# Performance work log

Hardware: AMD Instinct MI355X
Metric: run time of the kernel (lower is better)

The kernel has to match this reference:

```python
import jax, jax.numpy as jnp
import numpy as np

B, L, D, P = 2, 1024, 256, 32

def setup_inputs() -> dict:
    key = jax.random.key(0)
    k1, k2, k3, k4, k5 = jax.random.split(key, 5)
    x = jax.random.normal(k1, (B, L, D), dtype=jnp.float32)
    s_in = 1.0 / np.sqrt(D)
    W_phase = jax.random.normal(k2, (D, P), dtype=jnp.float32) * s_in
    b_phase = jax.random.normal(k3, (P,), dtype=jnp.float32) * 0.01
    W_val = jax.random.normal(k4, (D, D), dtype=jnp.float32) * s_in
    b_val = jax.random.normal(k5, (D,), dtype=jnp.float32) * 0.01
    return {"x": x, "W_phase": W_phase, "b_phase": b_phase, "W_val": W_val, "b_val": b_val}

def reference(x, W_phase, b_phase, W_val, b_val):
    # phases: [B, L, P] in (-pi, pi)
    phases = jnp.tanh(x @ W_phase + b_phase) * jnp.float32(np.pi)
    # unit-magnitude complex phasors: [B, L, P]
    phasors = jnp.exp(1j * phases)  # complex64
    # values: [B, L, D]
    values = x @ W_val + b_val
    # bind value vector to each phasor via outer product: [B, L, P, D] complex64
    bound = phasors[..., None] * values[:, :, None, :].astype(jnp.complex64)
    # holographic memory = running sum over sequence position
    memory = jnp.cumsum(bound, axis=1)
    return (memory, phases, phasors)
```

## Files before the change

kernel.cpp:

```cpp
#include <hip/hip_runtime.h>
#include <math.h>

#define B_ 2
#define L_ 1024
#define D_ 256
#define P_ 32
#define NROW (B_*L_)
#define C_ 16
#define CL_ (L_/C_)
#define PIF 3.14159265358979323846f

typedef float nvf4 __attribute__((ext_vector_type(4)));
typedef float nvf2 __attribute__((ext_vector_type(2)));

__global__ __launch_bounds__(256) void k_proj3(
    const float* __restrict__ x, const float* __restrict__ Wp,
    const float* __restrict__ bp, const float* __restrict__ Wv,
    const float* __restrict__ bv, float* __restrict__ values,
    float* __restrict__ phases_out, float* __restrict__ phasor_out,
    float* __restrict__ phasorT, int phasorMode, int mode, int hasPT)
{
    __shared__ float smem[2560];
    const int tid = threadIdx.x;

    if (blockIdx.x < NROW / 2) {
        const int row0 = blockIdx.x * 2;
        float*  xsv = smem;
        float4* red = (float4*)(smem + 512);

        if (tid < 128)
            ((float4*)xsv)[tid] = ((const float4*)(x + (size_t)row0 * D_))[tid];
        __syncthreads();

        const int q  = tid >> 6;
        const int c4 = tid & 63;
        const float4* Wv4 = (const float4*)Wv;
        float4 acc0 = make_float4(0.f, 0.f, 0.f, 0.f);
        float4 acc1 = make_float4(0.f, 0.f, 0.f, 0.f);

        const int k0 = q * 64;
        for (int kk = 0; kk < 64; kk += 4) {
            const int k = k0 + kk;
            float4 w0 = Wv4[(k + 0) * 64 + c4];
            float4 w1 = Wv4[(k + 1) * 64 + c4];
            float4 w2 = Wv4[(k + 2) * 64 + c4];
            float4 w3 = Wv4[(k + 3) * 64 + c4];
            float4 xa = *(const float4*)(xsv + 0 * D_ + k);
            float4 xb = *(const float4*)(xsv + 1 * D_ + k);
            acc0.x += xa.x*w0.x + xa.y*w1.x + xa.z*w2.x + xa.w*w3.x;
            acc0.y += xa.x*w0.y + xa.y*w1.y + xa.z*w2.y + xa.w*w3.y;
            acc0.z += xa.x*w0.z + xa.y*w1.z + xa.z*w2.z + xa.w*w3.z;
            acc0.w += xa.x*w0.w + xa.y*w1.w + xa.z*w2.w + xa.w*w3.w;
            acc1.x += xb.x*w0.x + xb.y*w1.x + xb.z*w2.x + xb.w*w3.x;
            acc1.y += xb.x*w0.y + xb.y*w1.y + xb.z*w2.y + xb.w*w3.y;
            acc1.z += xb.x*w0.z + xb.y*w1.z + xb.z*w2.z + xb.w*w3.z;
            acc1.w += xb.x*w0.w + xb.y*w1.w + xb.z*w2.w + xb.w*w3.w;
        }
        red[(0 * 4 + q) * 64 + c4] = acc0;
        red[(1 * 4 + q) * 64 + c4] = acc1;
        __syncthreads();

        if (tid < 128) {
            const int r2 = tid >> 6;
            const int cb = tid & 63;
            float4 s0 = red[(r2 * 4 + 0) * 64 + cb];
            float4 s1 = red[(r2 * 4 + 1) * 64 + cb];
            float4 s2 = red[(r2 * 4 + 2) * 64 + cb];
            float4 s3 = red[(r2 * 4 + 3) * 64 + cb];
            const float4 b4 = ((const float4*)bv)[cb];
            float4 o;
            o.x = s0.x + s1.x + s2.x + s3.x + b4.x;
            o.y = s0.y + s1.y + s2.y + s3.y + b4.y;
            o.z = s0.z + s1.z + s2.z + s3.z + b4.z;
            o.w = s0.w + s1.w + s2.w + s3.w + b4.w;
            ((float4*)values)[(size_t)(row0 + r2) * 64 + cb] = o;
        }
    } else {
        const int row0 = (blockIdx.x - NROW / 2) * 8;
        float* xs = smem;
        const float4* xg4 = (const float4*)(x + (size_t)row0 * D_);
        ((float4*)xs)[tid]       = xg4[tid];
        ((float4*)xs)[tid + 256] = xg4[tid + 256];
        __syncthreads();

        const int p  = tid & (P_ - 1);
        const int rr = tid >> 5;
        const float* xr = xs + rr * D_;
        float a0 = 0.f, a1 = 0.f, a2 = 0.f, a3 = 0.f;
        for (int k = 0; k < D_; k += 8) {
            float w0 = Wp[(k + 0) * P_ + p];
            float w1 = Wp[(k + 1) * P_ + p];
            float w2 = Wp[(k + 2) * P_ + p];
            float w3 = Wp[(k + 3) * P_ + p];
            float w4 = Wp[(k + 4) * P_ + p];
            float w5 = Wp[(k + 5) * P_ + p];
            float w6 = Wp[(k + 6) * P_ + p];
            float w7 = Wp[(k + 7) * P_ + p];
            float4 xA = *(const float4*)(xr + k);
            float4 xB = *(const float4*)(xr + k + 4);
            a0 += xA.x * w0; a1 += xA.y * w1; a2 += xA.z * w2; a3 += xA.w * w3;
            a0 += xB.x * w4; a1 += xB.y * w5; a2 += xB.z * w6; a3 += xB.w * w7;
        }
        float a = (a0 + a1) + (a2 + a3) + bp[p];
        float e  = __expf(2.0f * a);
        float ph = (1.0f - __fdividef(2.0f, e + 1.0f)) * PIF;
        const int row = row0 + rr;
        const int idx = row * P_ + p;
        phases_out[idx] = ph;
        float s, c;
        __sincosf(ph, &s, &c);
        if (phasorMode == 0) {
            ((float2*)phasor_out)[idx] = make_float2(c, s);
        } else if (phasorMode == 1) {
            phasor_out[idx] = c;
        }
        if (hasPT) {
            const int b = row >> 10, l = row & (L_ - 1);
            const size_t ti = (size_t)(b * P_ + p) * L_ + l;
            if (mode == 1) phasorT[ti] = c;
            else ((float2*)phasorT)[ti] = make_float2(c, s);
        }
    }
}

__global__ __launch_bounds__(128) void k_partial(
    const float* __restrict__ values, const float* __restrict__ phases,
    const float* __restrict__ phasorT, float* __restrict__ S,
    int mode, int hasPT)
{
    const int blk = blockIdx.x;
    const int c = blk & (C_ - 1);
    const int p = (blk >> 4) & (P_ - 1);
    const int b = blk >> 9;
    const int tid = threadIdx.x;
    const int l0 = c * CL_;
    const int bp = b * P_ + p;

    __shared__ float pcs[2 * CL_];
    if (hasPT) {
        if (mode == 1) {
            if (tid < CL_ / 4)
                ((float4*)pcs)[tid] =
                    ((const float4*)(phasorT + (size_t)bp * L_ + l0))[tid];
        } else {
            if (tid < CL_ / 2)
                ((float4*)pcs)[tid] = ((const float4*)
                    ((const float2*)phasorT + (size_t)bp * L_ + l0))[tid];
        }
    } else {
        if (tid < CL_) {
            float ph = phases[(b * L_ + l0 + tid) * P_ + p];
            if (mode == 1) pcs[tid] = __cosf(ph);
            else ((float2*)pcs)[tid] = make_float2(__cosf(ph), __sinf(ph));
        }
    }
    __syncthreads();

    const float2* vp = (const float2*)(values + (size_t)(b * L_ + l0) * D_) + tid;

    if (mode == 1) {
        float sx = 0.f, sy = 0.f;
        #pragma unroll
        for (int i = 0; i < CL_; ++i) {
            float pc = pcs[i];
            float2 v = vp[(size_t)i * (D_/2)];
            sx += pc * v.x;
            sy += pc * v.y;
        }
        ((float2*)S)[((size_t)bp * C_ + c) * (D_/2) + tid] = make_float2(sx, sy);
    } else {
        float4 a = make_float4(0.f, 0.f, 0.f, 0.f);
        #pragma unroll
        for (int i = 0; i < CL_; ++i) {
            float2 q = ((float2*)pcs)[i];
            float2 v = vp[(size_t)i * (D_/2)];
            a.x += q.x * v.x; a.y += q.y * v.x;
            a.z += q.x * v.y; a.w += q.y * v.y;
        }
        ((float4*)S)[((size_t)bp * C_ + c) * (D_/2) + tid] = a;
    }
}

__global__ __launch_bounds__(128) void k_scan(
    const float* __restrict__ values, const float* __restrict__ phases,
    const float* __restrict__ phasorT, const float* __restrict__ S,
    float* __restrict__ mem, int mode, int hasPT)
{
    const int blk = blockIdx.x;
    const int c = blk & (C_ - 1);
    const int p = (blk >> 4) & (P_ - 1);
    const int b = blk >> 9;
    const int tid = threadIdx.x;
    const int l0 = c * CL_;
    const int bp = b * P_ + p;

    __shared__ float pcs[2 * CL_];
    if (hasPT) {
        if (mode == 1) {
            if (tid < CL_ / 4)
                ((float4*)pcs)[tid] =
                    ((const float4*)(phasorT + (size_t)bp * L_ + l0))[tid];
        } else {
            if (tid < CL_ / 2)
                ((float4*)pcs)[tid] = ((const float4*)
                    ((const float2*)phasorT + (size_t)bp * L_ + l0))[tid];
        }
    } else {
        if (tid < CL_) {
            float ph = phases[(b * L_ + l0 + tid) * P_ + p];
            if (mode == 1) pcs[tid] = __cosf(ph);
            else ((float2*)pcs)[tid] = make_float2(__cosf(ph), __sinf(ph));
        }
    }

    const float2* vp = (const float2*)(values + (size_t)(b * L_ + l0) * D_) + tid;

    if (mode == 1) {
        float cx = 0.f, cz = 0.f;
        const float2* Sb = (const float2*)S + (size_t)bp * C_ * (D_/2) + tid;
        for (int cc = 0; cc < c; ++cc) {
            float2 s = Sb[(size_t)cc * (D_/2)];
            cx += s.x; cz += s.y;
        }
        __syncthreads();
        nvf2* dst = (nvf2*)mem + ((size_t)(b * L_ + l0) * P_ + p) * (D_/2) + tid;
        const size_t st = (size_t)P_ * (D_/2);
        #pragma unroll
        for (int i = 0; i < CL_; ++i) {
            float pc = pcs[i];
            float2 v = vp[(size_t)i * (D_/2)];
            cx += pc * v.x;
            cz += pc * v.y;
            nvf2 o = { cx, cz };
            __builtin_nontemporal_store(o, dst + (size_t)i * st);
        }
    } else {
        float4 carry = make_float4(0.f, 0.f, 0.f, 0.f);
        const float4* Sb = (const float4*)S + (size_t)bp * C_ * (D_/2) + tid;
        for (int cc = 0; cc < c; ++cc) {
            float4 s = Sb[(size_t)cc * (D_/2)];
            carry.x += s.x; carry.y += s.y; carry.z += s.z; carry.w += s.w;
        }
        __syncthreads();
        nvf4* dst = (nvf4*)mem + ((size_t)(b * L_ + l0) * P_ + p) * (D_/2) + tid;
        const size_t st = (size_t)P_ * (D_/2);
        #pragma unroll
        for (int i = 0; i < CL_; ++i) {
            float2 q = ((float2*)pcs)[i];
            float2 v = vp[(size_t)i * (D_/2)];
            carry.x += q.x * v.x; carry.y += q.y * v.x;
            carry.z += q.x * v.y; carry.w += q.y * v.y;
            nvf4 o = { carry.x, carry.y, carry.z, carry.w };
            __builtin_nontemporal_store(o, dst + (size_t)i * st);
        }
    }
}

__global__ __launch_bounds__(128) void k_scan_rc(
    const float* __restrict__ values, const float* __restrict__ phases,
    float* __restrict__ mem, int mode)
{
    const int blk = blockIdx.x;
    const int c = blk & (C_ - 1);
    const int p = (blk >> 4) & (P_ - 1);
    const int b = blk >> 9;
    const int tid = threadIdx.x;
    const int l0 = c * CL_;

    const float2* vb = (const float2*)(values + (size_t)b * L_ * D_);
    float4 carry = make_float4(0.f, 0.f, 0.f, 0.f);
    for (int l = 0; l < l0; ++l) {
        float ph = phases[(b * L_ + l) * P_ + p];
        float s = __sinf(ph), cs = __cosf(ph);
        float2 v = vb[l * (D_/2) + tid];
        carry.x += cs * v.x; carry.y += s * v.x;
        carry.z += cs * v.y; carry.w += s * v.y;
    }
    for (int i = 0; i < CL_; ++i) {
        const int l = l0 + i;
        float ph = phases[(b * L_ + l) * P_ + p];
        float s = __sinf(ph), cs = __cosf(ph);
        float2 v = vb[l * (D_/2) + tid];
        carry.x += cs * v.x; carry.y += s * v.x;
        carry.z += cs * v.y; carry.w += s * v.y;
        const size_t rowIdx = (size_t)(b * L_ + l) * P_ + p;
        if (mode == 0) ((float4*)mem)[rowIdx * (D_/2) + tid] = carry;
        else ((float2*)mem)[rowIdx * (D_/2) + tid] = make_float2(carry.x, carry.z);
    }
}

extern "C" void kernel_launch(void* const* d_in, const int* in_sizes, int n_in,
                              void* d_out, int out_size, void* d_ws, size_t ws_size,
                              hipStream_t stream) {
    const float* x  = (const float*)d_in[0];
    const float* Wp = (const float*)d_in[1];
    const float* bp = (const float*)d_in[2];
    const float* Wv = (const float*)d_in[3];
    const float* bv = (const float*)d_in[4];
    float* out = (float*)d_out;

    const size_t nMemF = (size_t)2 * B_ * L_ * P_ * D_;
    const size_t nMemR = (size_t)B_ * L_ * P_ * D_;
    const size_t nPh   = (size_t)B_ * L_ * P_;

    int mode; size_t memFloats;
    if ((size_t)out_size >= nMemF + 3 * nPh) { mode = 0; memFloats = nMemF; }
    else                                     { mode = 1; memFloats = nMemR; }
    const bool memFits      = (size_t)out_size >= memFloats;
    const bool phasesInOut  = (size_t)out_size >= memFloats + nPh;
    const bool phasorsInOut =
        (size_t)out_size >= memFloats + nPh + (mode == 0 ? 2 * nPh : nPh);

    const size_t valB = (size_t)B_ * L_ * D_ * sizeof(float);
    const size_t phB  = nPh * sizeof(float);
    const size_t sB   = (size_t)B_ * P_ * C_ * (D_/2) * sizeof(float4);
    const size_t ptB  = nPh * (mode == 0 ? sizeof(float2) : sizeof(float));
    float* values   = (float*)d_ws;
    float* phasesWs = (float*)((char*)d_ws + valB);
    float* S        = (float*)((char*)d_ws + valB + phB);
    float* phasorT  = (float*)((char*)d_ws + valB + phB + sB);

    float* phasesPtr = phasesInOut ? (out + memFloats)
                     : (ws_size >= valB + phB ? phasesWs : nullptr);
    if (phasesPtr == nullptr) return;

    float* phasorPtr = phasorsInOut ? (out + memFloats + nPh) : nullptr;
    const int phasorMode = phasorsInOut ? mode : 2;

    const bool pathA = ws_size >= valB + phB + sB;
    const int  hasPT = (pathA && ws_size >= valB + phB + sB + ptB) ? 1 : 0;

    k_proj3<<<NROW / 2 + NROW / 8, 256, 0, stream>>>(
        x, Wp, bp, Wv, bv, values, phasesPtr, phasorPtr, phasorT,
        phasorMode, mode, hasPT);
    if (!memFits) return;

    if (pathA) {
        k_partial<<<B_ * P_ * C_, 128, 0, stream>>>(values, phasesPtr, phasorT,
                                                    S, mode, hasPT);
        k_scan<<<B_ * P_ * C_, 128, 0, stream>>>(values, phasesPtr, phasorT,
                                                 S, out, mode, hasPT);
    } else {
        k_scan_rc<<<B_ * P_ * C_, 128, 0, stream>>>(values, phasesPtr, out, mode);
    }
}
```

Measured before the change: 107.9 us.

## Coalesce transposed phasor stores and add value-reusing chunk partial-sum kernel

The projection kernel now stages the cos/sin results in shared memory and writes the transposed phasor array as contiguous float4 runs per phase, where before each thread wrote a scattered element. A new partial-sum kernel loads one chunk of values and the phasors for all 32 phases into shared memory once. Each thread then accumulates over several phases and channels, so values are reused across phases instead of being re-read from global memory by one block per phase. This cuts grid size and global traffic, in exchange for more shared memory, an added barrier in the projection kernel and fewer, larger blocks.

```diff
diff --git a/kernel.cpp b/kernel.cpp
--- a/kernel.cpp
+++ b/kernel.cpp
@@ -13,6 +13,7 @@
 typedef float nvf4 __attribute__((ext_vector_type(4)));
 typedef float nvf2 __attribute__((ext_vector_type(2)));
 
+
 __global__ __launch_bounds__(256) void k_proj3(
     const float* __restrict__ x, const float* __restrict__ Wp,
     const float* __restrict__ bp, const float* __restrict__ Wv,
@@ -20,7 +21,7 @@
     float* __restrict__ phases_out, float* __restrict__ phasor_out,
     float* __restrict__ phasorT, int phasorMode, int mode, int hasPT)
 {
-    __shared__ float smem[2560];
+    __shared__ float smem[3072];
     const int tid = threadIdx.x;
 
     if (blockIdx.x < NROW / 2) {
@@ -115,18 +116,118 @@
             phasor_out[idx] = c;
         }
         if (hasPT) {
-            const int b = row >> 10, l = row & (L_ - 1);
-            const size_t ti = (size_t)(b * P_ + p) * L_ + l;
-            if (mode == 1) phasorT[ti] = c;
-            else ((float2*)phasorT)[ti] = make_float2(c, s);
-        }
+            const int bq    = row0 >> 10;
+            const int row0l = row0 & (L_ - 1);
+            if (mode == 1) {
+                float* ct = xs + 2048;
+                ct[p * 9 + rr] = c;
+                __syncthreads();
+                if (tid < 32) {
+                    const float* sp = ct + tid * 9;
+                    float4 A  = { sp[0], sp[1], sp[2], sp[3] };
+                    float4 Bv = { sp[4], sp[5], sp[6], sp[7] };
+                    float4* dst = (float4*)(phasorT +
+                        ((size_t)(bq * P_ + tid)) * L_ + row0l);
+                    dst[0] = A; dst[1] = Bv;
+                }
+            } else {
+                float2* ct2 = (float2*)(xs + 2048);
+                ct2[p * 9 + rr] = make_float2(c, s);
+                __syncthreads();
+                if (tid < 32) {
+                    const float2* sp = ct2 + tid * 9;
+                    float4* dst = (float4*)((float2*)phasorT +
+                        ((size_t)(bq * P_ + tid)) * L_ + row0l);
+                    dst[0] = make_float4(sp[0].x, sp[0].y, sp[1].x, sp[1].y);
+                    dst[1] = make_float4(sp[2].x, sp[2].y, sp[3].x, sp[3].y);
+                    dst[2] = make_float4(sp[4].x, sp[4].y, sp[5].x, sp[5].y);
+                    dst[3] = make_float4(sp[6].x, sp[6].y, sp[7].x, sp[7].y);
+                }
+            }
+        }
+    }
+}
+
+__global__ __launch_bounds__(256) void k_partial2(
+    const float* __restrict__ values, const float* __restrict__ phasorT,
+    float* __restrict__ S, int mode)
+{
+    const int blk = blockIdx.x;
+    const int ds  = blk & 7;
+    const int c   = (blk >> 3) & (C_ - 1);
+    const int b   = blk >> 7;
+    const int tid = threadIdx.x;
+    const int l0  = c * CL_;
+
+    __shared__ float smem2[2048 + 64 * 33 * 2];
+    float2* vs   = (float2*)smem2;
+    float*  pcs  = smem2 + 2048;
+    float2* pcs2 = (float2*)(smem2 + 2048);
+
+    const float2* vg = (const float2*)values;
+    #pragma unroll
+    for (int k = 0; k < 4; ++k) {
+        const int lin = tid + k * 256;
+        const int i = lin >> 4, jj = lin & 15;
+        vs[i * 16 + jj] =
+            vg[(size_t)(b * L_ + l0 + i) * (D_/2) + ds * 16 + jj];
+    }
+    if (mode == 1) {
+        #pragma unroll
+        for (int k = 0; k < 8; ++k) {
+            const int lin = tid + k * 256;
+            const int p = lin >> 6, i = lin & 63;
+            pcs[i * 33 + p] = phasorT[((size_t)b * P_ + p) * L_ + l0 + i];
+        }
+    } else {
+        #pragma unroll
+        for (int k = 0; k < 8; ++k) {
+            const int lin = tid + k * 256;
+            const int p = lin >> 6, i = lin & 63;
+            pcs2[i * 33 + p] =
+                ((const float2*)phasorT)[((size_t)b * P_ + p) * L_ + l0 + i];
+        }
+    }
+    __syncthreads();
+
+    const int p  = tid >> 3;
+    const int cp = tid & 7;
+
+    if (mode == 1) {
+        float sx0 = 0.f, sy0 = 0.f, sx1 = 0.f, sy1 = 0.f;
+        #pragma unroll 8
+        for (int i = 0; i < CL_; ++i) {
+            float  pc = pcs[i * 33 + p];
+            float2 v0 = vs[i * 16 + cp * 2];
+            float2 v1 = vs[i * 16 + cp * 2 + 1];
+            sx0 += pc * v0.x; sy0 += pc * v0.y;
+            sx1 += pc * v1.x; sy1 += pc * v1.y;
+        }
+        float4 o = make_float4(sx0, sy0, sx1, sy1);
+        ((float4*)S)[((size_t)(b * P_ + p) * C_ + c) * 64 + ds * 8 + cp] = o;
+    } else {
+        float4 a0 = make_float4(0.f,0.f,0.f,0.f);
+        float4 a1 = make_float4(0.f,0.f,0.f,0.f);
+        #pragma unroll 8
+        for (int i = 0; i < CL_; ++i) {
+            float2 q  = pcs2[i * 33 + p];
+            float2 v0 = vs[i * 16 + cp * 2];
+            float2 v1 = vs[i * 16 + cp * 2 + 1];
+            a0.x += q.x * v0.x; a0.y += q.y * v0.x;
+            a0.z += q.x * v0.y; a0.w += q.y * v0.y;
+            a1.x += q.x * v1.x; a1.y += q.y * v1.x;
+            a1.z += q.x * v1.y; a1.w += q.y * v1.y;
+        }
+        const size_t base =
+            ((size_t)(b * P_ + p) * C_ + c) * (D_/2) + ds * 16 + cp * 2;
+        ((float4*)S)[base]     = a0;
+        ((float4*)S)[base + 1] = a1;
     }
 }
 
 __global__ __launch_bounds__(128) void k_partial(
     const float* __restrict__ values, const float* __restrict__ phases,
-    const float* __restrict__ phasorT, float* __restrict__ S,
-    int mode, int hasPT)
+    float* __restrict__ S, int mode)
 {
     const int blk = blockIdx.x;
     const int c = blk & (C_ - 1);
@@ -137,22 +238,10 @@
     const int bp = b * P_ + p;
 
     __shared__ float pcs[2 * CL_];
-    if (hasPT) {
-        if (mode == 1) {
-            if (tid < CL_ / 4)
-                ((float4*)pcs)[tid] =
-                    ((const float4*)(phasorT + (size_t)bp * L_ + l0))[tid];
-        } else {
-            if (tid < CL_ / 2)
-                ((float4*)pcs)[tid] = ((const float4*)
-                    ((const float2*)phasorT + (size_t)bp * L_ + l0))[tid];
-        }
-    } else {
-        if (tid < CL_) {
-            float ph = phases[(b * L_ + l0 + tid) * P_ + p];
-            if (mode == 1) pcs[tid] = __cosf(ph);
-            else ((float2*)pcs)[tid] = make_float2(__cosf(ph), __sinf(ph));
-        }
+    if (tid < CL_) {
+        float ph = phases[(b * L_ + l0 + tid) * P_ + p];
+        if (mode == 1) pcs[tid] = __cosf(ph);
+        else ((float2*)pcs)[tid] = make_float2(__cosf(ph), __sinf(ph));
     }
     __syncthreads();
 
@@ -336,8 +425,11 @@
     if (!memFits) return;
 
     if (pathA) {
-        k_partial<<<B_ * P_ * C_, 128, 0, stream>>>(values, phasesPtr, phasorT,
-                                                    S, mode, hasPT);
+        if (hasPT) {
+            k_partial2<<<B_ * C_ * 8, 256, 0, stream>>>(values, phasorT, S, mode);
+        } else {
+            k_partial<<<B_ * P_ * C_, 128, 0, stream>>>(values, phasesPtr, S, mode);
+        }
         k_scan<<<B_ * P_ * C_, 128, 0, stream>>>(values, phasesPtr, phasorT,
                                                  S, out, mode, hasPT);
     } else {
```

Result: no change. 108.0 us (+0.0%).

## Fuse chunk-partial and scan kernels into one block-local two-pass scan

Applied to the files above, without the earlier changes.

Replaces the separate partial-sum and scan kernels with a single kernel. Each block owns one (batch, phase) pair and a 16-column slice of D, and it computes chunk partials into shared memory, then does an in-block carry prefix before writing the cumulative outputs. The projection kernel also stages phasor values in shared memory so the transposed phasor stores are vectorised and coalesced. This removes one launch and the global round trip of the partial sums, at the cost of fewer, larger blocks (512 instead of 1024) and more shared memory.

```diff
diff --git a/kernel.cpp b/kernel.cpp
--- a/kernel.cpp
+++ b/kernel.cpp
@@ -13,6 +13,7 @@
 typedef float nvf4 __attribute__((ext_vector_type(4)));
 typedef float nvf2 __attribute__((ext_vector_type(2)));
 
+
 __global__ __launch_bounds__(256) void k_proj3(
     const float* __restrict__ x, const float* __restrict__ Wp,
     const float* __restrict__ bp, const float* __restrict__ Wv,
@@ -20,7 +21,7 @@
     float* __restrict__ phases_out, float* __restrict__ phasor_out,
     float* __restrict__ phasorT, int phasorMode, int mode, int hasPT)
 {
-    __shared__ float smem[2560];
+    __shared__ float smem[3072];
     const int tid = threadIdx.x;
 
     if (blockIdx.x < NROW / 2) {
@@ -115,139 +116,136 @@
             phasor_out[idx] = c;
         }
         if (hasPT) {
-            const int b = row >> 10, l = row & (L_ - 1);
-            const size_t ti = (size_t)(b * P_ + p) * L_ + l;
-            if (mode == 1) phasorT[ti] = c;
-            else ((float2*)phasorT)[ti] = make_float2(c, s);
+            const int bq    = row0 >> 10;
+            const int row0l = row0 & (L_ - 1);
+            if (mode == 1) {
+                float* ct = xs + 2048;
+                ct[p * 9 + rr] = c;
+                __syncthreads();
+                if (tid < 32) {
+                    const float* sp = ct + tid * 9;
+                    float4 A  = { sp[0], sp[1], sp[2], sp[3] };
+                    float4 Bv = { sp[4], sp[5], sp[6], sp[7] };
+                    float4* dst = (float4*)(phasorT +
+                        ((size_t)(bq * P_ + tid)) * L_ + row0l);
+                    dst[0] = A; dst[1] = Bv;
+                }
+            } else {
+                float2* ct2 = (float2*)(xs + 2048);
+                ct2[p * 9 + rr] = make_float2(c, s);
+                __syncthreads();
+                if (tid < 32) {
+                    const float2* sp = ct2 + tid * 9;
+                    float4* dst = (float4*)((float2*)phasorT +
+                        ((size_t)(bq * P_ + tid)) * L_ + row0l);
+                    dst[0] = make_float4(sp[0].x, sp[0].y, sp[1].x, sp[1].y);
+                    dst[1] = make_float4(sp[2].x, sp[2].y, sp[3].x, sp[3].y);
+                    dst[2] = make_float4(sp[4].x, sp[4].y, sp[5].x, sp[5].y);
+                    dst[3] = make_float4(sp[6].x, sp[6].y, sp[7].x, sp[7].y);
+                }
+            }
         }
     }
 }
 
-__global__ __launch_bounds__(128) void k_partial(
+__global__ __launch_bounds__(256) void k_pscan(
     const float* __restrict__ values, const float* __restrict__ phases,
-    const float* __restrict__ phasorT, float* __restrict__ S,
+    const float* __restrict__ phasorT, float* __restrict__ mem,
     int mode, int hasPT)
 {
-    const int blk = blockIdx.x;
-    const int c = blk & (C_ - 1);
-    const int p = (blk >> 4) & (P_ - 1);
-    const int b = blk >> 9;
-    const int tid = threadIdx.x;
-    const int l0 = c * CL_;
-    const int bp = b * P_ + p;
-
-    __shared__ float pcs[2 * CL_];
+    const int blk  = blockIdx.x;
+    const int d8   = blk & 7;
+    const int p    = (blk >> 3) & (P_ - 1);
+    const int b    = blk >> 8;
+    const int tid  = threadIdx.x;
+    const int col  = tid & 15;
+    const int slot = tid >> 4;
+    const int bp   = b * P_ + p;
+    const int l0   = slot * CL_;
+
+    __shared__ float sm[3072];
+    float*  pcs   = sm;
+    float2* pcs2  = (float2*)sm;
+    float2* part2 = (float2*)(sm + 1024);
+    float4* part4 = (float4*)(sm + 2048);
+
     if (hasPT) {
         if (mode == 1) {
-            if (tid < CL_ / 4)
-                ((float4*)pcs)[tid] =
-                    ((const float4*)(phasorT + (size_t)bp * L_ + l0))[tid];
+            ((float4*)pcs)[tid] =
+                ((const float4*)(phasorT + (size_t)bp * L_))[tid];
         } else {
-            if (tid < CL_ / 2)
-                ((float4*)pcs)[tid] = ((const float4*)
-                    ((const float2*)phasorT + (size_t)bp * L_ + l0))[tid];
+            const float4* src =
+                (const float4*)((const float2*)phasorT + (size_t)bp * L_);
+            ((float4*)pcs2)[tid]       = src[tid];
+            ((float4*)pcs2)[tid + 256] = src[tid + 256];
         }
     } else {
-        if (tid < CL_) {
-            float ph = phases[(b * L_ + l0 + tid) * P_ + p];
-            if (mode == 1) pcs[tid] = __cosf(ph);
-            else ((float2*)pcs)[tid] = make_float2(__cosf(ph), __sinf(ph));
+        for (int l = tid; l < L_; l += 256) {
+            float ph = phases[(b * L_ + l) * P_ + p];
+            if (mode == 1) pcs[l] = __cosf(ph);
+            else           pcs2[l] = make_float2(__cosf(ph), __sinf(ph));
         }
     }
     __syncthreads();
 
-    const float2* vp = (const float2*)(values + (size_t)(b * L_ + l0) * D_) + tid;
+    const float2* vbase =
+        (const float2*)values + (size_t)(b * L_) * (D_/2) + d8 * 16 + col;
 
     if (mode == 1) {
         float sx = 0.f, sy = 0.f;
-        #pragma unroll
+        #pragma unroll 8
         for (int i = 0; i < CL_; ++i) {
-            float pc = pcs[i];
-            float2 v = vp[(size_t)i * (D_/2)];
+            float  pc = pcs[l0 + i];
+            float2 v  = vbase[(size_t)(l0 + i) * (D_/2)];
             sx += pc * v.x;
             sy += pc * v.y;
         }
-        ((float2*)S)[((size_t)bp * C_ + c) * (D_/2) + tid] = make_float2(sx, sy);
-    } else {
-        float4 a = make_float4(0.f, 0.f, 0.f, 0.f);
-        #pragma unroll
+        part2[slot * 16 + col] = make_float2(sx, sy);
+        __syncthreads();
+
+        float cx = 0.f, cz = 0.f;
+        for (int cc = 0; cc < slot; ++cc) {
+            float2 s = part2[cc * 16 + col];
+            cx += s.x; cz += s.y;
+        }
+
+        nvf2* dst = (nvf2*)mem +
+            ((size_t)(b * L_ + l0) * P_ + p) * (D_/2) + d8 * 16 + col;
+        const size_t st = (size_t)P_ * (D_/2);
+        #pragma unroll 8
         for (int i = 0; i < CL_; ++i) {
-            float2 q = ((float2*)pcs)[i];
-            float2 v = vp[(size_t)i * (D_/2)];
-            a.x += q.x * v.x; a.y += q.y * v.x;
-            a.z += q.x * v.y; a.w += q.y * v.y;
-        }
-        ((float4*)S)[((size_t)bp * C_ + c) * (D_/2) + tid] = a;
-    }
-}
-
-__global__ __launch_bounds__(128) void k_scan(
-    const float* __restrict__ values, const float* __restrict__ phases,
-    const float* __restrict__ phasorT, const float* __restrict__ S,
-    float* __restrict__ mem, int mode, int hasPT)
-{
-    const int blk = blockIdx.x;
-    const int c = blk & (C_ - 1);
-    const int p = (blk >> 4) & (P_ - 1);
-    const int b = blk >> 9;
-    const int tid = threadIdx.x;
-    const int l0 = c * CL_;
-    const int bp = b * P_ + p;
-
-    __shared__ float pcs[2 * CL_];
-    if (hasPT) {
-        if (mode == 1) {
-            if (tid < CL_ / 4)
-                ((float4*)pcs)[tid] =
-                    ((const float4*)(phasorT + (size_t)bp * L_ + l0))[tid];
-        } else {
-            if (tid < CL_ / 2)
-                ((float4*)pcs)[tid] = ((const float4*)
-                    ((const float2*)phasorT + (size_t)bp * L_ + l0))[tid];
-        }
-    } else {
-        if (tid < CL_) {
-            float ph = phases[(b * L_ + l0 + tid) * P_ + p];
-            if (mode == 1) pcs[tid] = __cosf(ph);
-            else ((float2*)pcs)[tid] = make_float2(__cosf(ph), __sinf(ph));
-        }
-    }
-
-    const float2* vp = (const float2*)(values + (size_t)(b * L_ + l0) * D_) + tid;
-
-    if (mode == 1) {
-        float cx = 0.f, cz = 0.f;
-        const float2* Sb = (const float2*)S + (size_t)bp * C_ * (D_/2) + tid;
-        for (int cc = 0; cc < c; ++cc) {
-            float2 s = Sb[(size_t)cc * (D_/2)];
-            cx += s.x; cz += s.y;
-        }
-        __syncthreads();
-        nvf2* dst = (nvf2*)mem + ((size_t)(b * L_ + l0) * P_ + p) * (D_/2) + tid;
-        const size_t st = (size_t)P_ * (D_/2);
-        #pragma unroll
-        for (int i = 0; i < CL_; ++i) {
-            float pc = pcs[i];
-            float2 v = vp[(size_t)i * (D_/2)];
+            float  pc = pcs[l0 + i];
+            float2 v  = vbase[(size_t)(l0 + i) * (D_/2)];
             cx += pc * v.x;
             cz += pc * v.y;
             nvf2 o = { cx, cz };
             __builtin_nontemporal_store(o, dst + (size_t)i * st);
         }
     } else {
+        float4 a = make_float4(0.f, 0.f, 0.f, 0.f);
+        #pragma unroll 8
+        for (int i = 0; i < CL_; ++i) {
+            float2 q = pcs2[l0 + i];
+            float2 v = vbase[(size_t)(l0 + i) * (D_/2)];
+            a.x += q.x * v.x; a.y += q.y * v.x;
+            a.z += q.x * v.y; a.w += q.y * v.y;
+        }
+        part4[slot * 16 + col] = a;
+        __syncthreads();
+
         float4 carry = make_float4(0.f, 0.f, 0.f, 0.f);
-        const float4* Sb = (const float4*)S + (size_t)bp * C_ * (D_/2) + tid;
-        for (int cc = 0; cc < c; ++cc) {
-            float4 s = Sb[(size_t)cc * (D_/2)];
+        for (int cc = 0; cc < slot; ++cc) {
+            float4 s = part4[cc * 16 + col];
             carry.x += s.x; carry.y += s.y; carry.z += s.z; carry.w += s.w;
         }
-        __syncthreads();
-        nvf4* dst = (nvf4*)mem + ((size_t)(b * L_ + l0) * P_ + p) * (D_/2) + tid;
+
+        nvf4* dst = (nvf4*)mem +
+            ((size_t)(b * L_ + l0) * P_ + p) * (D_/2) + d8 * 16 + col;
         const size_t st = (size_t)P_ * (D_/2);
-        #pragma unroll
+        #pragma unroll 8
         for (int i = 0; i < CL_; ++i) {
-            float2 q = ((float2*)pcs)[i];
-            float2 v = vp[(size_t)i * (D_/2)];
+            float2 q = pcs2[l0 + i];
+            float2 v = vbase[(size_t)(l0 + i) * (D_/2)];
             carry.x += q.x * v.x; carry.y += q.y * v.x;
             carry.z += q.x * v.y; carry.w += q.y * v.y;
             nvf4 o = { carry.x, carry.y, carry.z, carry.w };
@@ -317,7 +315,6 @@
     const size_t ptB  = nPh * (mode == 0 ? sizeof(float2) : sizeof(float));
     float* values   = (float*)d_ws;
     float* phasesWs = (float*)((char*)d_ws + valB);
-    float* S        = (float*)((char*)d_ws + valB + phB);
     float* phasorT  = (float*)((char*)d_ws + valB + phB + sB);
 
     float* phasesPtr = phasesInOut ? (out + memFloats)
@@ -327,8 +324,8 @@
     float* phasorPtr = phasorsInOut ? (out + memFloats + nPh) : nullptr;
     const int phasorMode = phasorsInOut ? mode : 2;
 
-    const bool pathA = ws_size >= valB + phB + sB;
-    const int  hasPT = (pathA && ws_size >= valB + phB + sB + ptB) ? 1 : 0;
+    const bool pathA = ws_size >= valB + phB;
+    const int  hasPT = (ws_size >= valB + phB + sB + ptB) ? 1 : 0;
 
     k_proj3<<<NROW / 2 + NROW / 8, 256, 0, stream>>>(
         x, Wp, bp, Wv, bv, values, phasesPtr, phasorPtr, phasorT,
@@ -336,10 +333,8 @@
     if (!memFits) return;
 
     if (pathA) {
-        k_partial<<<B_ * P_ * C_, 128, 0, stream>>>(values, phasesPtr, phasorT,
-                                                    S, mode, hasPT);
-        k_scan<<<B_ * P_ * C_, 128, 0, stream>>>(values, phasesPtr, phasorT,
-                                                 S, out, mode, hasPT);
+        k_pscan<<<B_ * P_ * 8, 256, 0, stream>>>(values, phasesPtr, phasorT,
+                                                 out, mode, hasPT);
     } else {
         k_scan_rc<<<B_ * P_ * C_, 128, 0, stream>>>(values, phasesPtr, out, mode);
     }
```

Result: faster. 104.6 us (-3.1%).
